# Kernel optimization log

Hardware: AMD Instinct MI355X
Metric: run time of the kernel (lower is better)

The kernel has to match this reference:

```python
import jax, jax.numpy as jnp
import numpy as np

CAPACITY_FACTOR = 1.25

def setup_inputs() -> dict:
    key = jax.random.key(0)
    ks = jax.random.split(key, 6)
    B, S, D, H, E = 4, 2048, 1024, 2048, 8
    x = jax.random.normal(ks[0], (B, S, D), dtype=jnp.float32)
    Wg = jax.random.normal(ks[1], (D, E), dtype=jnp.float32) / np.float32(np.sqrt(D))
    bg = jnp.zeros((E,), dtype=jnp.float32)
    W1 = jax.random.normal(ks[2], (E, H, D), dtype=jnp.float32) / np.float32(np.sqrt(H))
    W2 = jax.random.normal(ks[3], (E, D, H), dtype=jnp.float32) / np.float32(np.sqrt(D))
    W3 = jax.random.normal(ks[4], (E, D, H), dtype=jnp.float32) / np.float32(np.sqrt(D))
    return {"x": x, "Wg": Wg, "bg": bg, "W1": W1, "W2": W2, "W3": W3, "deterministic": 1}


def reference(x, Wg, bg, W1, W2, W3, deterministic):
    # deterministic=True path: no gate noise, no dropout (rate=0 anyway).
    b, s, d = x.shape
    E = W1.shape[0]
    xt = x.reshape(-1, d)                      # [N, d]
    N = xt.shape[0]
    cap = int(N / E * CAPACITY_FACTOR)

    logits = xt @ Wg + bg                      # [N, E]
    eid = jnp.argmax(logits, axis=1)           # [N] assigned expert (top-1)
    onehot = jax.nn.one_hot(eid, E, dtype=xt.dtype)
    # 0-based arrival position of each token within its expert's queue
    pos = (jnp.sum(jnp.cumsum(onehot, axis=0) * onehot, axis=1)).astype(jnp.int32) - 1
    valid = pos < cap                          # capacity mask (pos >= 0 always)
    slot = jnp.where(valid, pos, cap)          # overflow tokens -> dummy slot `cap`

    # Dispatch: scatter tokens into [E, cap+1, d]; slots unique among valid tokens
    buf = jnp.zeros((E, cap + 1, d), dtype=xt.dtype).at[eid, slot].set(xt)
    binp = buf[:, :cap]                        # [E, cap, d] (dummy slot dropped)

    # Grouped SwiGLU FFN per expert
    h = jax.nn.silu(jnp.einsum('ecd,edh->ech', binp, W2)) * jnp.einsum('ecd,edh->ech', binp, W3)
    bout = jnp.einsum('ech,ehd->ecd', h, W1)   # [E, cap, d]

    # Combine: gather each token's expert output; overflow tokens read zero row
    bout = jnp.concatenate([bout, jnp.zeros((E, 1, d), dtype=bout.dtype)], axis=1)
    eout = bout[eid, slot]                     # [N, d]

    weights = jax.nn.softmax(logits, axis=-1)
    gate_w = jnp.take_along_axis(weights, eid[:, None], axis=1)  # [N, 1]
    out = (gate_w * eout).reshape(b, s, d)
    return out
```

## Files before the change

kernel.cpp:

```cpp
#include <hip/hip_runtime.h>

#define N_TOK 8192
#define D_DIM 1024
#define H_DIM 2048
#define E_NUM 8
#define CAP   1280

typedef __attribute__((ext_vector_type(8))) short bf16x8;
typedef __attribute__((ext_vector_type(4))) float f32x4;

__device__ inline unsigned short f2bf(float f) {
  unsigned u = __float_as_uint(f);
  u += 0x7fffu + ((u >> 16) & 1u);
  return (unsigned short)(u >> 16);
}

#define VMCNT(n) asm volatile("s_waitcnt vmcnt(" #n ")" ::: "memory")
#define BARRIER() asm volatile("s_barrier" ::: "memory")

__global__ __launch_bounds__(256) void transpose_cvt_all(const float* __restrict__ W2,
                                                         const float* __restrict__ W3,
                                                         const float* __restrict__ W1,
                                                         unsigned short* __restrict__ w2t,
                                                         unsigned short* __restrict__ w3t,
                                                         unsigned short* __restrict__ w1t) {
  __shared__ float tile[64][33];
  const int id = blockIdx.x;
  const float* src;
  unsigned short* dst;
  int R, C, bx, by, b;
  if (id < 16384) {
    const int q = id & 8191;
    b = q >> 10;
    const int rem = q & 1023;
    bx = rem & 63;
    by = rem >> 6;
    R = D_DIM; C = H_DIM;
    src = (id < 8192 ? W2 : W3);
    dst = (id < 8192 ? w2t : w3t);
  } else {
    const int q = id - 16384;
    b = q >> 10;
    const int rem = q & 1023;
    bx = rem & 31;
    by = rem >> 5;
    R = H_DIM; C = D_DIM;
    src = W1; dst = w1t;
  }
  src += (size_t)b * R * C;
  dst += (size_t)b * R * C;
  const int c0 = bx * 32, r0 = by * 64;
  const int tx = threadIdx.x & 31, ty = threadIdx.x >> 5;
#pragma unroll
  for (int i = 0; i < 8; ++i)
    tile[ty + i * 8][tx] = src[(size_t)(r0 + ty + i * 8) * C + c0 + tx];
  __syncthreads();
  const int rp = threadIdx.x & 31;
  const int cb = threadIdx.x >> 5;
#pragma unroll
  for (int it = 0; it < 4; ++it) {
    const int c = cb + it * 8;
    unsigned short v[2] = {f2bf(tile[2 * rp][c]), f2bf(tile[2 * rp + 1][c])};
    *reinterpret_cast<unsigned*>(dst + (size_t)(c0 + c) * R + r0 + 2 * rp) =
        *reinterpret_cast<unsigned*>(v);
  }
}

__global__ __launch_bounds__(256) void gate_kernel(const float* __restrict__ x,
                                                   const float* __restrict__ Wg,
                                                   const float* __restrict__ bg,
                                                   int* __restrict__ eid,
                                                   float* __restrict__ gatew) {
  __shared__ float wg[E_NUM][D_DIM];
  const int tid = threadIdx.x;
  for (int i = tid; i < D_DIM * E_NUM; i += 256) {
    int d = i >> 3, e = i & 7;
    wg[e][d] = Wg[i];
  }
  __syncthreads();
  const int w = tid >> 6, l = tid & 63;
  const int t = blockIdx.x * 4 + w;
  const float* xr = x + (size_t)t * D_DIM;
  float acc[8] = {0, 0, 0, 0, 0, 0, 0, 0};
#pragma unroll
  for (int i = 0; i < D_DIM / 64; ++i) {
    float xv = xr[l + 64 * i];
#pragma unroll
    for (int e = 0; e < 8; ++e) acc[e] += xv * wg[e][l + 64 * i];
  }
#pragma unroll
  for (int off = 32; off >= 1; off >>= 1) {
#pragma unroll
    for (int e = 0; e < 8; ++e) acc[e] += __shfl_xor(acc[e], off);
  }
  if (l == 0) {
    float best = -1e30f;
    int bi = 0;
#pragma unroll
    for (int e = 0; e < 8; ++e) {
      acc[e] += bg[e];
      if (acc[e] > best) { best = acc[e]; bi = e; }
    }
    float s = 0.f;
#pragma unroll
    for (int e = 0; e < 8; ++e) s += __expf(acc[e] - best);
    eid[t] = bi;
    gatew[t] = 1.f / s;
  }
}

__global__ void scan_kernel(const int* __restrict__ eid, int* __restrict__ slot,
                            int* __restrict__ tok_of) {
  __shared__ int se[N_TOK];
  const int tid = threadIdx.x;
  for (int i = tid; i < N_TOK; i += 256) se[i] = eid[i];
  __syncthreads();
  if (tid >= 64) return;
  int counts[8] = {0, 0, 0, 0, 0, 0, 0, 0};
  const unsigned long long lower = (tid == 0) ? 0ull : ((1ull << tid) - 1ull);
  for (int base = 0; base < N_TOK; base += 64) {
    const int t = base + tid;
    const int e = se[t];
    int rank = 0;
#pragma unroll
    for (int ee = 0; ee < 8; ++ee) {
      unsigned long long m = __ballot(e == ee);
      if (e == ee) rank = counts[ee] + __popcll(m & lower);
      counts[ee] += __popcll(m);
    }
    slot[t] = rank < CAP ? rank : CAP;
    if (rank < CAP) tok_of[e * CAP + rank] = t;
  }
}

__global__ __launch_bounds__(256) void scatter_kernel(const float* __restrict__ x,
                                                      const int* __restrict__ tok_of,
                                                      unsigned short* __restrict__ binp) {
  const int row = blockIdx.x * 4 + (threadIdx.x >> 6);
  const int l = threadIdx.x & 63;
  const int t = tok_of[row];
  unsigned short* dst = binp + (size_t)row * D_DIM;
  if (t >= 0) {
    const float* src = x + (size_t)t * D_DIM;
#pragma unroll
    for (int i = 0; i < 4; ++i) {
      const int d = (i * 64 + l) * 4;
      float4 v = *reinterpret_cast<const float4*>(src + d);
      unsigned short r[4] = {f2bf(v.x), f2bf(v.y), f2bf(v.z), f2bf(v.w)};
      *reinterpret_cast<uint2*>(dst + d) = *reinterpret_cast<uint2*>(r);
    }
  } else {
    uint2 z = {0u, 0u};
#pragma unroll
    for (int i = 0; i < 4; ++i) {
      const int d = (i * 64 + l) * 4;
      *reinterpret_cast<uint2*>(dst + d) = z;
    }
  }
}

#define TILE64 (128 * 64)

__device__ inline void stage_tile(const unsigned short* __restrict__ g, int ldg, int k0,
                                  unsigned short* lds, int w, int l) {
  const int gcol = (l & 7) ^ (l >> 3);
  const unsigned short* gsrc = g + (size_t)(w * 32 + (l >> 3)) * ldg + k0 + gcol * 8;
#pragma unroll
  for (int it = 0; it < 4; ++it) {
    __builtin_amdgcn_global_load_lds(
        (const __attribute__((address_space(1))) unsigned int*)(gsrc + (size_t)(it * 8) * ldg),
        (__attribute__((address_space(3))) unsigned int*)(lds + (w * 32 + it * 8) * 64),
        16, 0, 0);
  }
}

__device__ inline bf16x8 lds_frag(const unsigned short* lds, int row, int c16) {
  return *reinterpret_cast<const bf16x8*>(lds + row * 64 + (c16 ^ (row & 7)) * 8);
}

__global__ __launch_bounds__(256, 2) void ffn1_kernel(const unsigned short* __restrict__ binp,
                                                      const unsigned short* __restrict__ w2t,
                                                      const unsigned short* __restrict__ w3t,
                                                      unsigned short* __restrict__ hbuf) {
  __shared__ unsigned short sA[2][TILE64], sB2[TILE64], sB3[TILE64];
  const int id = (blockIdx.x & 7) * 160 + (blockIdx.x >> 3);
  const int e = id / 160;
  const int rem = id - e * 160;
  const int bx = rem / 10;
  const int by = rem - bx * 10;
  const unsigned short* A  = binp + (size_t)e * CAP * D_DIM + (size_t)by * 128 * D_DIM;
  const unsigned short* B2 = w2t + (size_t)e * H_DIM * D_DIM + (size_t)bx * 128 * D_DIM;
  const unsigned short* B3 = w3t + (size_t)e * H_DIM * D_DIM + (size_t)bx * 128 * D_DIM;
  unsigned short* H = hbuf + (size_t)e * CAP * H_DIM;
  const int tid = threadIdx.x;
  const int l = tid & 63;
  const int w = tid >> 6, wr = w >> 1, wc = w & 1;
  f32x4 acc2[4][4] = {};
  f32x4 acc3[4][4] = {};

  stage_tile(A, D_DIM, 0, sA[0], w, l);

  const int NT = D_DIM / 64;
  int cur = 0;
  for (int kt = 0; kt < NT; ++kt) {
    stage_tile(B2, D_DIM, kt * 64, sB2, w, l);
    stage_tile(B3, D_DIM, kt * 64, sB3, w, l);
    if (kt + 1 < NT) {
      stage_tile(A, D_DIM, (kt + 1) * 64, sA[cur ^ 1], w, l);
      VMCNT(4);
    } else {
      VMCNT(0);
    }
    BARRIER();
#pragma unroll
    for (int kk = 0; kk < 2; ++kk) {
      const int c16 = kk * 4 + (l >> 4);
      bf16x8 af[4], b2f[4], b3f[4];
#pragma unroll
      for (int f = 0; f < 4; ++f) {
        af[f]  = lds_frag(sA[cur], wr * 64 + f * 16 + (l & 15), c16);
        b2f[f] = lds_frag(sB2, wc * 64 + f * 16 + (l & 15), c16);
        b3f[f] = lds_frag(sB3, wc * 64 + f * 16 + (l & 15), c16);
      }
#pragma unroll
      for (int fm = 0; fm < 4; ++fm)
#pragma unroll
        for (int fn = 0; fn < 4; ++fn) {
          acc2[fm][fn] = __builtin_amdgcn_mfma_f32_16x16x32_bf16(af[fm], b2f[fn], acc2[fm][fn], 0, 0, 0);
          acc3[fm][fn] = __builtin_amdgcn_mfma_f32_16x16x32_bf16(af[fm], b3f[fn], acc3[fm][fn], 0, 0, 0);
        }
    }
    BARRIER();
    cur ^= 1;
  }

  const int row0 = by * 128 + wr * 64;
  const int col0 = bx * 128 + wc * 64;
#pragma unroll
  for (int fm = 0; fm < 4; ++fm)
#pragma unroll
    for (int fn = 0; fn < 4; ++fn)
#pragma unroll
      for (int j = 0; j < 4; ++j) {
        const int row = row0 + fm * 16 + (l >> 4) * 4 + j;
        const int col = col0 + fn * 16 + (l & 15);
        const float v2 = acc2[fm][fn][j];
        const float v3 = acc3[fm][fn][j];
        const float hv = (v2 / (1.0f + __expf(-v2))) * v3;
        H[(size_t)row * H_DIM + col] = f2bf(hv);
      }
}

__global__ __launch_bounds__(256, 2) void ffn2_kernel(const unsigned short* __restrict__ hbuf,
                                                      const unsigned short* __restrict__ w1t,
                                                      const int* __restrict__ tok_of,
                                                      const float* __restrict__ gatew,
                                                      float* __restrict__ out) {
  __shared__ unsigned short sA[2][TILE64], sB[TILE64];
  const int id = (blockIdx.x & 7) * 80 + (blockIdx.x >> 3);
  const int e = id / 80;
  const int rem = id - e * 80;
  const int bx = rem / 10;
  const int by = rem - bx * 10;
  const unsigned short* A = hbuf + (size_t)e * CAP * H_DIM + (size_t)by * 128 * H_DIM;
  const unsigned short* B = w1t + (size_t)e * D_DIM * H_DIM + (size_t)bx * 128 * H_DIM;
  const int* tok = tok_of + e * CAP;
  const int tid = threadIdx.x;
  const int l = tid & 63;
  const int w = tid >> 6, wr = w >> 1, wc = w & 1;
  f32x4 acc[4][4] = {};

  stage_tile(A, H_DIM, 0, sA[0], w, l);

  const int NT = H_DIM / 64;
  int cur = 0;
  for (int kt = 0; kt < NT; ++kt) {
    stage_tile(B, H_DIM, kt * 64, sB, w, l);
    if (kt + 1 < NT) {
      stage_tile(A, H_DIM, (kt + 1) * 64, sA[cur ^ 1], w, l);
      VMCNT(4);
    } else {
      VMCNT(0);
    }
    BARRIER();
#pragma unroll
    for (int kk = 0; kk < 2; ++kk) {
      const int c16 = kk * 4 + (l >> 4);
      bf16x8 af[4], bfr[4];
#pragma unroll
      for (int f = 0; f < 4; ++f) {
        af[f]  = lds_frag(sA[cur], wr * 64 + f * 16 + (l & 15), c16);
        bfr[f] = lds_frag(sB, wc * 64 + f * 16 + (l & 15), c16);
      }
#pragma unroll
      for (int fm = 0; fm < 4; ++fm)
#pragma unroll
        for (int fn = 0; fn < 4; ++fn)
          acc[fm][fn] = __builtin_amdgcn_mfma_f32_16x16x32_bf16(af[fm], bfr[fn], acc[fm][fn], 0, 0, 0);
    }
    BARRIER();
    cur ^= 1;
  }

  const int row0 = by * 128 + wr * 64;
  const int col0 = bx * 128 + wc * 64;
#pragma unroll
  for (int fm = 0; fm < 4; ++fm)
#pragma unroll
    for (int j = 0; j < 4; ++j) {
      const int row = row0 + fm * 16 + (l >> 4) * 4 + j;
      const int t = tok[row];
      if (t >= 0) {
        const float g = gatew[t];
#pragma unroll
        for (int fn = 0; fn < 4; ++fn) {
          const int col = col0 + fn * 16 + (l & 15);
          out[(size_t)t * D_DIM + col] = g * acc[fm][fn][j];
        }
      }
    }
}

__global__ __launch_bounds__(256) void zero_overflow(const int* __restrict__ slot,
                                                     float* __restrict__ out) {
  const int t = blockIdx.x * 4 + (threadIdx.x >> 6);
  if (slot[t] < CAP) return;
  const int l = threadIdx.x & 63;
  float4 z = {0.f, 0.f, 0.f, 0.f};
#pragma unroll
  for (int i = 0; i < 4; ++i)
    *reinterpret_cast<float4*>(out + (size_t)t * D_DIM + (i * 64 + l) * 4) = z;
}

extern "C" void kernel_launch(void* const* d_in, const int* in_sizes, int n_in,
                              void* d_out, int out_size, void* d_ws, size_t ws_size,
                              hipStream_t stream) {
  const float* x  = (const float*)d_in[0];
  const float* Wg = (const float*)d_in[1];
  const float* bg = (const float*)d_in[2];
  const float* W1 = (const float*)d_in[3];
  const float* W2 = (const float*)d_in[4];
  const float* W3 = (const float*)d_in[5];
  float* out = (float*)d_out;

  char* ws = (char*)d_ws;
  unsigned short* w2t = (unsigned short*)ws; ws += (size_t)E_NUM * H_DIM * D_DIM * 2;
  unsigned short* w3t = (unsigned short*)ws; ws += (size_t)E_NUM * H_DIM * D_DIM * 2;
  unsigned short* w1t = (unsigned short*)ws; ws += (size_t)E_NUM * D_DIM * H_DIM * 2;
  unsigned short* binp = (unsigned short*)ws; ws += (size_t)E_NUM * CAP * D_DIM * 2;
  unsigned short* hbuf = (unsigned short*)ws; ws += (size_t)E_NUM * CAP * H_DIM * 2;
  int* eid = (int*)ws;    ws += (size_t)N_TOK * 4;
  float* gw = (float*)ws; ws += (size_t)N_TOK * 4;
  int* slot = (int*)ws;   ws += (size_t)N_TOK * 4;
  int* tok_of = (int*)ws; ws += (size_t)E_NUM * CAP * 4;

  transpose_cvt_all<<<24576, 256, 0, stream>>>(W2, W3, W1, w2t, w3t, w1t);
  hipMemsetAsync(tok_of, 0xFF, (size_t)E_NUM * CAP * 4, stream);
  gate_kernel<<<N_TOK / 4, 256, 0, stream>>>(x, Wg, bg, eid, gw);
  scan_kernel<<<1, 256, 0, stream>>>(eid, slot, tok_of);
  scatter_kernel<<<E_NUM * CAP / 4, 256, 0, stream>>>(x, tok_of, binp);
  ffn1_kernel<<<1280, 256, 0, stream>>>(binp, w2t, w3t, hbuf);
  ffn2_kernel<<<640, 256, 0, stream>>>(hbuf, w1t, tok_of, gw, out);
  zero_overflow<<<N_TOK / 4, 256, 0, stream>>>(slot, out);
}
```

Before: 256.2 us.

## Load A fragments directly to registers and double-buffer weight tiles in LDS

Both FFN GEMM kernels now load the activation (A) operand straight from global memory into register fragments instead of staging it through LDS. The freed LDS is used to double-buffer the weight (B) tiles, and the K loop is unrolled by two with ping-pong register and LDS buffers. This removes the LDS round-trip and the ds_reads for A and lets the next tile's loads overlap compute. The cost is more VGPRs for two sets of A fragments, which with launch_bounds(256,2) may cause spills. The A loads also lose the coalescing that the LDS staging path gave, and the hand-set vmcnt waits depend on the exact number of loads in flight.

```diff
diff --git a/kernel.cpp b/kernel.cpp
--- a/kernel.cpp
+++ b/kernel.cpp
@@ -178,11 +178,40 @@
   return *reinterpret_cast<const bf16x8*>(lds + row * 64 + (c16 ^ (row & 7)) * 8);
 }
 
+#define LOAD_A_FFN1(dst, kt)                                                       \
+  {                                                                                \
+    _Pragma("unroll") for (int kk = 0; kk < 2; ++kk)                               \
+        _Pragma("unroll") for (int f = 0; f < 4; ++f)                              \
+            dst[kk * 4 + f] = *reinterpret_cast<const bf16x8*>(                    \
+                aBase + (size_t)f * 16 * D_DIM + (kt) * 64 + kk * 32);             \
+  }
+
+#define FFN1_COMPUTE(aX, ib)                                                       \
+  {                                                                                \
+    _Pragma("unroll") for (int kk = 0; kk < 2; ++kk) {                             \
+      const int c16 = kk * 4 + (l >> 4);                                           \
+      bf16x8 b2f[4], b3f[4];                                                       \
+      _Pragma("unroll") for (int f = 0; f < 4; ++f) {                              \
+        b2f[f] = lds_frag(sB2[ib], wc * 64 + f * 16 + (l & 15), c16);              \
+        b3f[f] = lds_frag(sB3[ib], wc * 64 + f * 16 + (l & 15), c16);              \
+      }                                                                            \
+      _Pragma("unroll") for (int fm = 0; fm < 4; ++fm)                             \
+          _Pragma("unroll") for (int fn = 0; fn < 4; ++fn) {                       \
+        acc2[fm][fn] = __builtin_amdgcn_mfma_f32_16x16x32_bf16(aX[kk * 4 + fm],    \
+                                                               b2f[fn],            \
+                                                               acc2[fm][fn], 0, 0, 0); \
+        acc3[fm][fn] = __builtin_amdgcn_mfma_f32_16x16x32_bf16(aX[kk * 4 + fm],    \
+                                                               b3f[fn],            \
+                                                               acc3[fm][fn], 0, 0, 0); \
+      }                                                                            \
+    }                                                                              \
+  }
+
 __global__ __launch_bounds__(256, 2) void ffn1_kernel(const unsigned short* __restrict__ binp,
                                                       const unsigned short* __restrict__ w2t,
                                                       const unsigned short* __restrict__ w3t,
                                                       unsigned short* __restrict__ hbuf) {
-  __shared__ unsigned short sA[2][TILE64], sB2[TILE64], sB3[TILE64];
+  __shared__ unsigned short sB2[2][TILE64], sB3[2][TILE64];
   const int id = (blockIdx.x & 7) * 160 + (blockIdx.x >> 3);
   const int e = id / 160;
   const int rem = id - e * 160;
@@ -195,43 +224,34 @@
   const int tid = threadIdx.x;
   const int l = tid & 63;
   const int w = tid >> 6, wr = w >> 1, wc = w & 1;
+  const unsigned short* aBase = A + (size_t)(wr * 64 + (l & 15)) * D_DIM + (l >> 4) * 8;
   f32x4 acc2[4][4] = {};
   f32x4 acc3[4][4] = {};
-
-  stage_tile(A, D_DIM, 0, sA[0], w, l);
-
-  const int NT = D_DIM / 64;
-  int cur = 0;
-  for (int kt = 0; kt < NT; ++kt) {
-    stage_tile(B2, D_DIM, kt * 64, sB2, w, l);
-    stage_tile(B3, D_DIM, kt * 64, sB3, w, l);
-    if (kt + 1 < NT) {
-      stage_tile(A, D_DIM, (kt + 1) * 64, sA[cur ^ 1], w, l);
-      VMCNT(4);
+  bf16x8 aE[8], aO[8];
+
+  stage_tile(B2, D_DIM, 0, sB2[0], w, l);
+  stage_tile(B3, D_DIM, 0, sB3[0], w, l);
+  LOAD_A_FFN1(aE, 0);
+
+  for (int kt = 0; kt < 16; kt += 2) {
+    stage_tile(B2, D_DIM, (kt + 1) * 64, sB2[1], w, l);
+    stage_tile(B3, D_DIM, (kt + 1) * 64, sB3[1], w, l);
+    LOAD_A_FFN1(aO, kt + 1);
+    VMCNT(16);
+    BARRIER();
+    FFN1_COMPUTE(aE, 0);
+    BARRIER();
+    if (kt + 2 < 16) {
+      stage_tile(B2, D_DIM, (kt + 2) * 64, sB2[0], w, l);
+      stage_tile(B3, D_DIM, (kt + 2) * 64, sB3[0], w, l);
+      LOAD_A_FFN1(aE, kt + 2);
+      VMCNT(16);
     } else {
       VMCNT(0);
     }
     BARRIER();
-#pragma unroll
-    for (int kk = 0; kk < 2; ++kk) {
-      const int c16 = kk * 4 + (l >> 4);
-      bf16x8 af[4], b2f[4], b3f[4];
-#pragma unroll
-      for (int f = 0; f < 4; ++f) {
-        af[f]  = lds_frag(sA[cur], wr * 64 + f * 16 + (l & 15), c16);
-        b2f[f] = lds_frag(sB2, wc * 64 + f * 16 + (l & 15), c16);
-        b3f[f] = lds_frag(sB3, wc * 64 + f * 16 + (l & 15), c16);
-      }
-#pragma unroll
-      for (int fm = 0; fm < 4; ++fm)
-#pragma unroll
-        for (int fn = 0; fn < 4; ++fn) {
-          acc2[fm][fn] = __builtin_amdgcn_mfma_f32_16x16x32_bf16(af[fm], b2f[fn], acc2[fm][fn], 0, 0, 0);
-          acc3[fm][fn] = __builtin_amdgcn_mfma_f32_16x16x32_bf16(af[fm], b3f[fn], acc3[fm][fn], 0, 0, 0);
-        }
-    }
-    BARRIER();
-    cur ^= 1;
+    FFN1_COMPUTE(aO, 1);
+    BARRIER();
   }
 
   const int row0 = by * 128 + wr * 64;
@@ -251,12 +271,34 @@
       }
 }
 
+#define LOAD_A_FFN2(dst, kt)                                                       \
+  {                                                                                \
+    _Pragma("unroll") for (int kk = 0; kk < 2; ++kk)                               \
+        _Pragma("unroll") for (int f = 0; f < 4; ++f)                              \
+            dst[kk * 4 + f] = *reinterpret_cast<const bf16x8*>(                    \
+                aBase + (size_t)f * 16 * H_DIM + (kt) * 64 + kk * 32);             \
+  }
+
+#define FFN2_COMPUTE(aX, ib)                                                       \
+  {                                                                                \
+    _Pragma("unroll") for (int kk = 0; kk < 2; ++kk) {                             \
+      const int c16 = kk * 4 + (l >> 4);                                           \
+      bf16x8 bfr[4];                                                               \
+      _Pragma("unroll") for (int f = 0; f < 4; ++f)                                \
+          bfr[f] = lds_frag(sB[ib], wc * 64 + f * 16 + (l & 15), c16);             \
+      _Pragma("unroll") for (int fm = 0; fm < 4; ++fm)                             \
+          _Pragma("unroll") for (int fn = 0; fn < 4; ++fn)                         \
+              acc[fm][fn] = __builtin_amdgcn_mfma_f32_16x16x32_bf16(               \
+                  aX[kk * 4 + fm], bfr[fn], acc[fm][fn], 0, 0, 0);                 \
+    }                                                                              \
+  }
+
 __global__ __launch_bounds__(256, 2) void ffn2_kernel(const unsigned short* __restrict__ hbuf,
                                                       const unsigned short* __restrict__ w1t,
                                                       const int* __restrict__ tok_of,
                                                       const float* __restrict__ gatew,
                                                       float* __restrict__ out) {
-  __shared__ unsigned short sA[2][TILE64], sB[TILE64];
+  __shared__ unsigned short sB[2][TILE64];
   const int id = (blockIdx.x & 7) * 80 + (blockIdx.x >> 3);
   const int e = id / 80;
   const int rem = id - e * 80;
@@ -268,38 +310,30 @@
   const int tid = threadIdx.x;
   const int l = tid & 63;
   const int w = tid >> 6, wr = w >> 1, wc = w & 1;
+  const unsigned short* aBase = A + (size_t)(wr * 64 + (l & 15)) * H_DIM + (l >> 4) * 8;
   f32x4 acc[4][4] = {};
-
-  stage_tile(A, H_DIM, 0, sA[0], w, l);
-
-  const int NT = H_DIM / 64;
-  int cur = 0;
-  for (int kt = 0; kt < NT; ++kt) {
-    stage_tile(B, H_DIM, kt * 64, sB, w, l);
-    if (kt + 1 < NT) {
-      stage_tile(A, H_DIM, (kt + 1) * 64, sA[cur ^ 1], w, l);
-      VMCNT(4);
+  bf16x8 aE[8], aO[8];
+
+  stage_tile(B, H_DIM, 0, sB[0], w, l);
+  LOAD_A_FFN2(aE, 0);
+
+  for (int kt = 0; kt < 32; kt += 2) {
+    stage_tile(B, H_DIM, (kt + 1) * 64, sB[1], w, l);
+    LOAD_A_FFN2(aO, kt + 1);
+    VMCNT(12);
+    BARRIER();
+    FFN2_COMPUTE(aE, 0);
+    BARRIER();
+    if (kt + 2 < 32) {
+      stage_tile(B, H_DIM, (kt + 2) * 64, sB[0], w, l);
+      LOAD_A_FFN2(aE, kt + 2);
+      VMCNT(12);
     } else {
       VMCNT(0);
     }
     BARRIER();
-#pragma unroll
-    for (int kk = 0; kk < 2; ++kk) {
-      const int c16 = kk * 4 + (l >> 4);
-      bf16x8 af[4], bfr[4];
-#pragma unroll
-      for (int f = 0; f < 4; ++f) {
-        af[f]  = lds_frag(sA[cur], wr * 64 + f * 16 + (l & 15), c16);
-        bfr[f] = lds_frag(sB, wc * 64 + f * 16 + (l & 15), c16);
-      }
-#pragma unroll
-      for (int fm = 0; fm < 4; ++fm)
-#pragma unroll
-        for (int fn = 0; fn < 4; ++fn)
-          acc[fm][fn] = __builtin_amdgcn_mfma_f32_16x16x32_bf16(af[fm], bfr[fn], acc[fm][fn], 0, 0, 0);
-    }
-    BARRIER();
-    cur ^= 1;
+    FFN2_COMPUTE(aO, 1);
+    BARRIER();
   }
 
   const int row0 = by * 128 + wr * 64;
```

Result: slower. 487.8 us (+90.4%).
